# Kernel tuning notes

Measured on AMD Instinct MI355X. Metric: run time of the kernel, lower is better.

Reference implementation:

```python
import jax, jax.numpy as jnp
import numpy as np

N = 50000
E = 600000
F_IN = 128      # float features (in_channels - 1)
CE = 8          # cell embedding dim
D_IN = F_IN + CE  # 136
C = 128         # out_channels
NUM_CELLS = 854
NEG_SLOPE = 0.2
LN_EPS = 1e-5


def _gat_layer(x, src, dst, W, a_src, a_dst, b):
    """PyG GATConv, heads=1, concat=False, add_self_loops already in src/dst.
    x: [N, Din]; src/dst: [Etot]; W: [Din, C]; a_src/a_dst: [C]; b: [C].
    """
    h = x @ W                               # [N, C]
    alpha_src = h @ a_src                   # [N]
    alpha_dst = h @ a_dst                   # [N]
    e = jax.nn.leaky_relu(alpha_src[src] + alpha_dst[dst], NEG_SLOPE)  # [Etot]
    # segment softmax over edges sharing a destination node
    m = jax.ops.segment_max(e, dst, num_segments=N)    # [N] (every node has a self-loop)
    ex = jnp.exp(e - m[dst])                           # [Etot]
    denom = jax.ops.segment_sum(ex, dst, num_segments=N)  # [N]
    alpha = ex / denom[dst]                            # [Etot]
    out = jax.ops.segment_sum(h[src] * alpha[:, None], dst, num_segments=N)  # [N, C]
    return out + b


def _layer_norm(x, g, b):
    mu = jnp.mean(x, axis=-1, keepdims=True)
    var = jnp.var(x, axis=-1, keepdims=True)
    return (x - mu) * jax.lax.rsqrt(var + LN_EPS) * g + b


def setup_inputs() -> dict:
    key = jax.random.key(0)
    ks = jax.random.split(key, 12)
    x_base = jax.random.normal(ks[0], (N, F_IN), dtype=jnp.float32)
    cell_ids = jax.random.randint(ks[1], (N,), 0, NUM_CELLS, dtype=jnp.int64)
    edge_index = jax.random.randint(ks[2], (2, E), 0, N, dtype=jnp.int64)
    s = 0.05
    cell_emb = jax.random.normal(ks[3], (NUM_CELLS, CE), dtype=jnp.float32)
    W1 = jax.random.normal(ks[4], (D_IN, C), dtype=jnp.float32) * s
    a_src1 = jax.random.normal(ks[5], (C,), dtype=jnp.float32) * s
    a_dst1 = jax.random.normal(ks[6], (C,), dtype=jnp.float32) * s
    b1 = jnp.zeros((C,), dtype=jnp.float32)
    ln_g = jnp.ones((C,), dtype=jnp.float32)
    ln_b = jnp.zeros((C,), dtype=jnp.float32)
    W2 = jax.random.normal(ks[7], (C, C), dtype=jnp.float32) * s
    a_src2 = jax.random.normal(ks[8], (C,), dtype=jnp.float32) * s
    a_dst2 = jax.random.normal(ks[9], (C,), dtype=jnp.float32) * s
    b2 = jnp.zeros((C,), dtype=jnp.float32)
    return {
        "x_base": x_base, "cell_ids": cell_ids, "edge_index": edge_index,
        "cell_emb": cell_emb,
        "W1": W1, "a_src1": a_src1, "a_dst1": a_dst1, "b1": b1,
        "ln_g": ln_g, "ln_b": ln_b,
        "W2": W2, "a_src2": a_src2, "a_dst2": a_dst2, "b2": b2,
    }


def reference(x_base, cell_ids, edge_index, cell_emb,
              W1, a_src1, a_dst1, b1, ln_g, ln_b,
              W2, a_src2, a_dst2, b2):
    # embed cell ids and concat (equiv. to x[:, :-1] + Embedding(x[:, -1]))
    x = jnp.concatenate([x_base, cell_emb[cell_ids]], axis=1)   # [N, 136]
    # PyG GATConv adds self-loops internally
    loops = jnp.arange(N, dtype=edge_index.dtype)
    src = jnp.concatenate([edge_index[0], loops])
    dst = jnp.concatenate([edge_index[1], loops])
    # layer 1 + LN + ELU (dropout inactive in eval mode)
    x = _gat_layer(x, src, dst, W1, a_src1, a_dst1, b1)
    x = jax.nn.elu(_layer_norm(x, ln_g, ln_b))
    # layer 2 (no norm/activation on last layer)
    x = _gat_layer(x, src, dst, W2, a_src2, a_dst2, b2)
    return x
```

## Files before the change

kernel.cpp:

```cpp
#include <hip/hip_runtime.h>
#include <hip/hip_fp16.h>
#include <cstdint>
#include <cstddef>

#define NEG_SLOPE 0.2f
#define LN_EPS 1e-5f

constexpr int BS = 256;
constexpr int EPT = 8;
constexpr int STRIDE = 96;

typedef _Float16 f16x8 __attribute__((ext_vector_type(8)));
typedef float f32x4 __attribute__((ext_vector_type(4)));

__global__ __launch_bounds__(256) void k_init(
    int* __restrict__ cnt, unsigned short* __restrict__ sn,
    const float* __restrict__ W1, const float* __restrict__ W2,
    _Float16* __restrict__ Wt1, _Float16* __restrict__ Wt2,
    int n, int nbN)
{
    int b = blockIdx.x;
    if (b < nbN) {
        int i = b * BS + threadIdx.x;
        if (i < n) { cnt[i] = 1; sn[(size_t)i * STRIDE] = (unsigned short)i; }
    } else {
        int idx = (b - nbN) * BS + threadIdx.x;
        if (idx < 128 * 160) {
            int nn = idx / 160, k = idx - nn * 160;
            Wt1[idx] = (_Float16)((k < 136) ? W1[(size_t)k * 128 + nn] : 0.f);
        } else if (idx < 128 * 160 + 128 * 128) {
            int j = idx - 128 * 160;
            int nn = j >> 7, k = j & 127;
            Wt2[j] = (_Float16)W2[(size_t)k * 128 + nn];
        }
    }
}

__global__ __launch_bounds__(256) void k_scatter_gemm1(
    const int* __restrict__ esrc, const int* __restrict__ edst,
    int* __restrict__ cnt, unsigned short* __restrict__ sn,
    const float* __restrict__ x, const int* __restrict__ cid,
    const float* __restrict__ emb,
    const _Float16* __restrict__ Wt1,
    const float* __restrict__ a_src, const float* __restrict__ a_dst,
    _Float16* __restrict__ hb, float* __restrict__ as_, float* __restrict__ ad_,
    int e, int n, int nbG, int nbA)
{
    __shared__ float red[2][16][2][2];
    int b = blockIdx.x;
    int role, idx;
    int nInter = 2 * (nbG < nbA ? nbG : nbA);
    if (b < nInter)      { role = b & 1; idx = b >> 1; }
    else if (nbG < nbA)  { role = 1; idx = (b - nInter) + nbG; }
    else                 { role = 0; idx = (b - nInter) + nbA; }

    if (role == 1) {
        int base = idx * (BS * EPT) + threadIdx.x;
        int sv[EPT], dv[EPT], slot[EPT];
        #pragma unroll
        for (int u = 0; u < EPT; ++u) {
            int i = base + u * BS;
            bool ok = i < e;
            int ii = ok ? i : 0;
            sv[u] = esrc[ii];
            dv[u] = ok ? edst[ii] : -1;
        }
        #pragma unroll
        for (int u = 0; u < EPT; ++u)
            slot[u] = (dv[u] >= 0) ? atomicAdd(&cnt[dv[u]], 1) : STRIDE;
        #pragma unroll
        for (int u = 0; u < EPT; ++u)
            if (slot[u] < STRIDE)
                sn[(size_t)dv[u] * STRIDE + slot[u]] = (unsigned short)sv[u];
        return;
    }

    int tid = threadIdx.x;
    int wave = tid >> 6, lane = tid & 63;
    int rg = wave >> 1, ch = wave & 1;
    int r15 = lane & 15, q = lane >> 4;
    int rowBase = idx * 32 + rg * 16;
    int colBase = ch * 64;
    int row = rowBase + r15;
    bool ok = row < n;
    int rl = ok ? row : n - 1;

    f32x4 acc[4] = {};
    const _Float16* Wp[4];
    #pragma unroll
    for (int s = 0; s < 4; ++s)
        Wp[s] = Wt1 + (size_t)(colBase + s * 16 + r15) * 160 + q * 8;
    const float* Xp = x + (size_t)rl * 128 + q * 8;

    #pragma unroll
    for (int k0 = 0; k0 < 128; k0 += 32) {
        f16x8 wv[4];
        #pragma unroll
        for (int s = 0; s < 4; ++s) wv[s] = *(const f16x8*)(Wp[s] + k0);
        float4 xlo = *(const float4*)(Xp + k0);
        float4 xhi = *(const float4*)(Xp + k0 + 4);
        f16x8 xv;
        xv[0] = (_Float16)xlo.x; xv[1] = (_Float16)xlo.y;
        xv[2] = (_Float16)xlo.z; xv[3] = (_Float16)xlo.w;
        xv[4] = (_Float16)xhi.x; xv[5] = (_Float16)xhi.y;
        xv[6] = (_Float16)xhi.z; xv[7] = (_Float16)xhi.w;
        #pragma unroll
        for (int s = 0; s < 4; ++s)
            acc[s] = __builtin_amdgcn_mfma_f32_16x16x32_f16(wv[s], xv, acc[s], 0, 0, 0);
    }
    {
        f16x8 wv[4];
        #pragma unroll
        for (int s = 0; s < 4; ++s) wv[s] = *(const f16x8*)(Wp[s] + 128);
        f16x8 xv;
        #pragma unroll
        for (int j = 0; j < 8; ++j) xv[j] = (_Float16)0.f;
        if (q == 0) {
            const float* er = emb + (size_t)cid[rl] * 8;
            float4 e0 = *(const float4*)er;
            float4 e1 = *(const float4*)(er + 4);
            xv[0] = (_Float16)e0.x; xv[1] = (_Float16)e0.y;
            xv[2] = (_Float16)e0.z; xv[3] = (_Float16)e0.w;
            xv[4] = (_Float16)e1.x; xv[5] = (_Float16)e1.y;
            xv[6] = (_Float16)e1.z; xv[7] = (_Float16)e1.w;
        }
        #pragma unroll
        for (int s = 0; s < 4; ++s)
            acc[s] = __builtin_amdgcn_mfma_f32_16x16x32_f16(wv[s], xv, acc[s], 0, 0, 0);
    }

    float vs = 0.f, vd = 0.f;
    #pragma unroll
    for (int s = 0; s < 4; ++s) {
        float4 as4 = *(const float4*)&a_src[colBase + s * 16 + q * 4];
        float4 ad4 = *(const float4*)&a_dst[colBase + s * 16 + q * 4];
        f32x4 d = acc[s];
        vs += d[0]*as4.x + d[1]*as4.y + d[2]*as4.z + d[3]*as4.w;
        vd += d[0]*ad4.x + d[1]*ad4.y + d[2]*ad4.z + d[3]*ad4.w;
        if (ok) {
            ushort4 u;
            u.x = __half_as_ushort(__float2half_rn(d[0]));
            u.y = __half_as_ushort(__float2half_rn(d[1]));
            u.z = __half_as_ushort(__float2half_rn(d[2]));
            u.w = __half_as_ushort(__float2half_rn(d[3]));
            *(ushort4*)&hb[(size_t)row * 128 + colBase + s * 16 + q * 4] = u;
        }
    }
    vs += __shfl_xor(vs, 16); vs += __shfl_xor(vs, 32);
    vd += __shfl_xor(vd, 16); vd += __shfl_xor(vd, 32);
    if (q == 0) { red[rg][r15][ch][0] = vs; red[rg][r15][ch][1] = vd; }
    __syncthreads();
    if (ch == 0 && q == 0 && ok) {
        as_[row] = red[rg][r15][0][0] + red[rg][r15][1][0];
        ad_[row] = red[rg][r15][0][1] + red[rg][r15][1][1];
    }
}

__global__ __launch_bounds__(512, 8) void k_agg1_gemm2(
    const _Float16* __restrict__ h1, const unsigned short* __restrict__ sn,
    const int* __restrict__ cnt, const float* __restrict__ as1,
    const float* __restrict__ ad1, const float* __restrict__ b1,
    const float* __restrict__ lng, const float* __restrict__ lnb,
    const _Float16* __restrict__ Wt2,
    const float* __restrict__ a_src2, const float* __restrict__ a_dst2,
    _Float16* __restrict__ h2, float* __restrict__ as2, float* __restrict__ ad2,
    int nn)
{
    __shared__ _Float16 yt[32][144];
    __shared__ float red[2][16][4][2];
    int t = blockIdx.x;
    int tid = threadIdx.x;
    int wave = tid >> 6, lane = tid & 63;
    int l4 = lane & 15, q = lane >> 4;
    int qg = wave * 4 + q;
    int node = t * 32 + qg;
    bool valid = node < nn;
    const char* hbB = (const char*)h1;

    int len = 0; float adv = 0.f;
    if (valid) {
        len = cnt[node];
        len = len < STRIDE ? len : STRIDE;
        adv = ad1[node];
    }
    int start = node * STRIDE;
    int sub = l4 & 3;

    float acc[8] = {0.f, 0.f, 0.f, 0.f, 0.f, 0.f, 0.f, 0.f};
    float dsum = 0.f;
    for (int j = 0; j < len; j += 4) {
        int rem = len - j;
        unsigned long long s4 = *(const unsigned long long*)(sn + start + j);
        int my = (int)((s4 >> (sub * 16)) & 0xFFFFull);
        float tt = as1[my] + adv;
        tt = tt > 0.f ? tt : NEG_SLOPE * tt;
        float w = __expf(fminf(tt, 70.f));
        #pragma unroll
        for (int i = 0; i < 4; ++i) {
            if (i < rem) {
                int si = (int)((s4 >> (i * 16)) & 0xFFFFull);
                float wi = __shfl(w, (lane & 48) | i);
                f16x8 hv = *(const f16x8*)(hbB + ((size_t)si << 8) + l4 * 16);
                #pragma unroll
                for (int c = 0; c < 8; ++c)
                    acc[c] = fmaf(wi, (float)hv[c], acc[c]);
                dsum += wi;
            }
        }
    }

    if (valid) {
        float inv = 1.f / dsum;
        float4 b0 = *(const float4*)&b1[l4 * 8];
        float4 bb = *(const float4*)&b1[l4 * 8 + 4];
        float vv[8];
        vv[0] = acc[0] * inv + b0.x; vv[1] = acc[1] * inv + b0.y;
        vv[2] = acc[2] * inv + b0.z; vv[3] = acc[3] * inv + b0.w;
        vv[4] = acc[4] * inv + bb.x; vv[5] = acc[5] * inv + bb.y;
        vv[6] = acc[6] * inv + bb.z; vv[7] = acc[7] * inv + bb.w;

        float s1 = 0.f, s2 = 0.f;
        #pragma unroll
        for (int c = 0; c < 8; ++c) { s1 += vv[c]; s2 += vv[c] * vv[c]; }
        #pragma unroll
        for (int o = 1; o < 16; o <<= 1) {
            s1 += __shfl_xor(s1, o);
            s2 += __shfl_xor(s2, o);
        }
        float mean = s1 * (1.f / 128.f);
        float var  = s2 * (1.f / 128.f) - mean * mean;
        float r = rsqrtf(var + LN_EPS);
        float4 g0 = *(const float4*)&lng[l4 * 8];
        float4 g1 = *(const float4*)&lng[l4 * 8 + 4];
        float4 p0 = *(const float4*)&lnb[l4 * 8];
        float4 p1 = *(const float4*)&lnb[l4 * 8 + 4];
        float gg[8] = {g0.x, g0.y, g0.z, g0.w, g1.x, g1.y, g1.z, g1.w};
        float pp[8] = {p0.x, p0.y, p0.z, p0.w, p1.x, p1.y, p1.z, p1.w};
        f16x8 o;
        #pragma unroll
        for (int c = 0; c < 8; ++c) {
            float u = (vv[c] - mean) * r * gg[c] + pp[c];
            u = u > 0.f ? u : __expf(u) - 1.f;
            o[c] = (_Float16)u;
        }
        *(f16x8*)&yt[qg][l4 * 8] = o;
    } else {
        f16x8 z;
        #pragma unroll
        for (int c = 0; c < 8; ++c) z[c] = (_Float16)0.f;
        *(f16x8*)&yt[qg][l4 * 8] = z;
    }
    __syncthreads();

    int rg = wave >> 2, cc = wave & 3;
    int r15 = l4;
    int row = t * 32 + rg * 16 + r15;
    bool ok = row < nn;

    f32x4 acc2[2] = {};
    const _Float16* Wp[2];
    #pragma unroll
    for (int s = 0; s < 2; ++s)
        Wp[s] = Wt2 + (size_t)(cc * 32 + s * 16 + r15) * 128 + q * 8;
    const _Float16* Yp = &yt[rg * 16 + r15][q * 8];

    #pragma unroll
    for (int k0 = 0; k0 < 128; k0 += 32) {
        f16x8 wv[2];
        #pragma unroll
        for (int s = 0; s < 2; ++s) wv[s] = *(const f16x8*)(Wp[s] + k0);
        f16x8 xv = *(const f16x8*)(Yp + k0);
        #pragma unroll
        for (int s = 0; s < 2; ++s)
            acc2[s] = __builtin_amdgcn_mfma_f32_16x16x32_f16(wv[s], xv, acc2[s], 0, 0, 0);
    }

    float vs = 0.f, vd = 0.f;
    #pragma unroll
    for (int s = 0; s < 2; ++s) {
        float4 as4 = *(const float4*)&a_src2[cc * 32 + s * 16 + q * 4];
        float4 ad4 = *(const float4*)&a_dst2[cc * 32 + s * 16 + q * 4];
        f32x4 d = acc2[s];
        vs += d[0]*as4.x + d[1]*as4.y + d[2]*as4.z + d[3]*as4.w;
        vd += d[0]*ad4.x + d[1]*ad4.y + d[2]*ad4.z + d[3]*ad4.w;
        if (ok) {
            ushort4 u;
            u.x = __half_as_ushort(__float2half_rn(d[0]));
            u.y = __half_as_ushort(__float2half_rn(d[1]));
            u.z = __half_as_ushort(__float2half_rn(d[2]));
            u.w = __half_as_ushort(__float2half_rn(d[3]));
            *(ushort4*)&h2[(size_t)row * 128 + cc * 32 + s * 16 + q * 4] = u;
        }
    }
    vs += __shfl_xor(vs, 16); vs += __shfl_xor(vs, 32);
    vd += __shfl_xor(vd, 16); vd += __shfl_xor(vd, 32);
    if (q == 0) { red[rg][r15][cc][0] = vs; red[rg][r15][cc][1] = vd; }
    __syncthreads();
    if (cc == 0 && q == 0 && ok) {
        as2[row] = red[rg][r15][0][0] + red[rg][r15][1][0]
                 + red[rg][r15][2][0] + red[rg][r15][3][0];
        ad2[row] = red[rg][r15][0][1] + red[rg][r15][1][1]
                 + red[rg][r15][2][1] + red[rg][r15][3][1];
    }
}

__global__ __launch_bounds__(256) void k_agg2(
    const _Float16* __restrict__ hb, const unsigned short* __restrict__ sn,
    const int* __restrict__ cnt, const float* __restrict__ as_,
    const float* __restrict__ ad_, const float* __restrict__ bias,
    float* __restrict__ out, int n_nodes)
{
    int tid = threadIdx.x;
    int wave = tid >> 6, lane = tid & 63;
    int l4 = lane & 15, q = lane >> 4;
    int node = blockIdx.x * 16 + wave * 4 + q;
    if (node >= n_nodes) return;
    int len = cnt[node];
    len = len < STRIDE ? len : STRIDE;
    int start = node * STRIDE;
    int sub = l4 & 3;
    float adv = ad_[node];
    const char* hbB = (const char*)hb;

    float acc[8] = {0.f, 0.f, 0.f, 0.f, 0.f, 0.f, 0.f, 0.f};
    float dsum = 0.f;
    for (int j = 0; j < len; j += 4) {
        int rem = len - j;
        unsigned long long s4 = *(const unsigned long long*)(sn + start + j);
        int my = (int)((s4 >> (sub * 16)) & 0xFFFFull);
        float t = as_[my] + adv;
        t = t > 0.f ? t : NEG_SLOPE * t;
        float w = __expf(fminf(t, 70.f));
        #pragma unroll
        for (int i = 0; i < 4; ++i) {
            if (i < rem) {
                int si = (int)((s4 >> (i * 16)) & 0xFFFFull);
                float wi = __shfl(w, (lane & 48) | i);
                f16x8 hv = *(const f16x8*)(hbB + ((size_t)si << 8) + l4 * 16);
                #pragma unroll
                for (int c = 0; c < 8; ++c)
                    acc[c] = fmaf(wi, (float)hv[c], acc[c]);
                dsum += wi;
            }
        }
    }

    float inv = 1.f / dsum;
    float4 b0 = *(const float4*)&bias[l4 * 8];
    float4 b1 = *(const float4*)&bias[l4 * 8 + 4];
    float4 o0 = make_float4(acc[0]*inv + b0.x, acc[1]*inv + b0.y,
                            acc[2]*inv + b0.z, acc[3]*inv + b0.w);
    float4 o1 = make_float4(acc[4]*inv + b1.x, acc[5]*inv + b1.y,
                            acc[6]*inv + b1.z, acc[7]*inv + b1.w);
    *(float4*)(out + (size_t)node * 128 + l4 * 8)     = o0;
    *(float4*)(out + (size_t)node * 128 + l4 * 8 + 4) = o1;
}


extern "C" void kernel_launch(void* const* d_in, const int* in_sizes, int n_in,
                              void* d_out, int out_size, void* d_ws, size_t ws_size,
                              hipStream_t stream) {
    const float* x_base   = (const float*)d_in[0];
    const int*   cell_ids = (const int*)d_in[1];
    const int*   eidx     = (const int*)d_in[2];
    const float* cell_emb = (const float*)d_in[3];
    const float* W1     = (const float*)d_in[4];
    const float* a_src1 = (const float*)d_in[5];
    const float* a_dst1 = (const float*)d_in[6];
    const float* b1     = (const float*)d_in[7];
    const float* ln_g   = (const float*)d_in[8];
    const float* ln_b   = (const float*)d_in[9];
    const float* W2     = (const float*)d_in[10];
    const float* a_src2 = (const float*)d_in[11];
    const float* a_dst2 = (const float*)d_in[12];
    const float* b2     = (const float*)d_in[13];

    const int N = in_sizes[0] / 128;
    const int E = in_sizes[2] / 2;

    const int* esrc = eidx;
    const int* edst = eidx + E;

    auto align = [](size_t v) { return (v + 255) & ~(size_t)255; };
    char* p = (char*)d_ws;
    int*   cnt    = (int*)p;   p += align((size_t)N * 4);
    unsigned short* sn = (unsigned short*)p; p += align((size_t)N * STRIDE * 2 + 64);
    _Float16* h1  = (_Float16*)p; p += align((size_t)N * 128 * 2);
    _Float16* h2  = (_Float16*)p; p += align((size_t)N * 128 * 2);
    _Float16* Wt1 = (_Float16*)p; p += align((size_t)128 * 160 * 2);
    _Float16* Wt2 = (_Float16*)p; p += align((size_t)128 * 128 * 2);
    float* as1    = (float*)p; p += align((size_t)N * 4);
    float* ad1    = (float*)p; p += align((size_t)N * 4);
    float* as2    = (float*)p; p += align((size_t)N * 4);
    float* ad2    = (float*)p; p += align((size_t)N * 4);
    (void)ws_size; (void)n_in; (void)out_size;

    const int nbN = (N + BS - 1) / BS;
    const int nbA = (E + BS * EPT - 1) / (BS * EPT);
    const int nbG = (N + 31) / 32;
    const int wblocks = (128 * 160 + 128 * 128 + BS - 1) / BS;

    k_init<<<nbN + wblocks, BS, 0, stream>>>(cnt, sn, W1, W2, Wt1, Wt2, N, nbN);
    k_scatter_gemm1<<<nbG + nbA, BS, 0, stream>>>(
        esrc, edst, cnt, sn, x_base, cell_ids, cell_emb, Wt1,
        a_src1, a_dst1, h1, as1, ad1, E, N, nbG, nbA);
    k_agg1_gemm2<<<nbG, 512, 0, stream>>>(
        h1, sn, cnt, as1, ad1, b1, ln_g, ln_b, Wt2,
        a_src2, a_dst2, h2, as2, ad2, N);
    k_agg2<<<(N + 15) / 16, BS, 0, stream>>>(
        h2, sn, cnt, as2, ad2, b2, (float*)d_out, N);
}
```

Baseline: 222.1 us.

## Replace global-atomic edge scatter with two-pass bucketed CSR build using shared atomics

Edge-to-adjacency construction changes from one pass of global atomicAdd per edge into a two-pass bucket sort. The first pass bins edges by destination into 1024-node buckets per edge block using LDS atomics and writes packed (dst_local, src) words. The second pass has one block per bucket fill the per-node slot lists with shared-memory counters. This removes contended global atomics, but each sub-bucket is capped at 96 entries, so edges can be dropped silently if a block sends more than 96 edges to one bucket. Bucket-building blocks now run serially over about 293 sub-lists per bucket, which may become a long tail.

```diff
diff --git a/kernel.cpp b/kernel.cpp
--- a/kernel.cpp
+++ b/kernel.cpp
@@ -8,23 +8,49 @@
 
 constexpr int BS = 256;
 constexpr int EPT = 8;
+constexpr int SUBCAP = 96;
 constexpr int STRIDE = 96;
 
 typedef _Float16 f16x8 __attribute__((ext_vector_type(8)));
 typedef float f32x4 __attribute__((ext_vector_type(4)));
 
 __global__ __launch_bounds__(256) void k_init(
-    int* __restrict__ cnt, unsigned short* __restrict__ sn,
+    const int* __restrict__ esrc, const int* __restrict__ edst,
+    unsigned int* __restrict__ gb, int* __restrict__ bcnt,
     const float* __restrict__ W1, const float* __restrict__ W2,
     _Float16* __restrict__ Wt1, _Float16* __restrict__ Wt2,
-    int n, int nbN)
+    int e, int nb, int nblk)
 {
     int b = blockIdx.x;
-    if (b < nbN) {
-        int i = b * BS + threadIdx.x;
-        if (i < n) { cnt[i] = 1; sn[(size_t)i * STRIDE] = (unsigned short)i; }
+    if (b < nblk) {
+        __shared__ int lcnt[64];
+        int tid = threadIdx.x;
+        if (tid < 64) lcnt[tid] = 0;
+        __syncthreads();
+        int base = b * (BS * EPT) + tid;
+        int sv[EPT], dl[EPT], bk[EPT], lp[EPT];
+        #pragma unroll
+        for (int u = 0; u < EPT; ++u) {
+            int i = base + u * BS;
+            bool ok = i < e;
+            int ii = ok ? i : 0;
+            sv[u] = esrc[ii];
+            int d = edst[ii];
+            dl[u] = d & 1023;
+            bk[u] = ok ? (d >> 10) : -1;
+        }
+        #pragma unroll
+        for (int u = 0; u < EPT; ++u)
+            lp[u] = (bk[u] >= 0) ? atomicAdd(&lcnt[bk[u]], 1) : SUBCAP;
+        __syncthreads();
+        if (tid < nb) bcnt[b * nb + tid] = lcnt[tid] < SUBCAP ? lcnt[tid] : SUBCAP;
+        #pragma unroll
+        for (int u = 0; u < EPT; ++u)
+            if (bk[u] >= 0 && lp[u] < SUBCAP)
+                gb[((size_t)bk[u] * nblk + b) * SUBCAP + lp[u]] =
+                    ((unsigned)dl[u] << 16) | (unsigned)sv[u];
     } else {
-        int idx = (b - nbN) * BS + threadIdx.x;
+        int idx = (b - nblk) * BS + threadIdx.x;
         if (idx < 128 * 160) {
             int nn = idx / 160, k = idx - nn * 160;
             Wt1[idx] = (_Float16)((k < 136) ? W1[(size_t)k * 128 + nn] : 0.f);
@@ -36,45 +62,49 @@
     }
 }
 
-__global__ __launch_bounds__(256) void k_scatter_gemm1(
-    const int* __restrict__ esrc, const int* __restrict__ edst,
+__global__ __launch_bounds__(256) void k_csr_gemm1(
+    const unsigned int* __restrict__ gb, const int* __restrict__ bcnt,
     int* __restrict__ cnt, unsigned short* __restrict__ sn,
     const float* __restrict__ x, const int* __restrict__ cid,
     const float* __restrict__ emb,
     const _Float16* __restrict__ Wt1,
     const float* __restrict__ a_src, const float* __restrict__ a_dst,
     _Float16* __restrict__ hb, float* __restrict__ as_, float* __restrict__ ad_,
-    int e, int n, int nbG, int nbA)
+    int n, int nb, int nblk)
 {
     __shared__ float red[2][16][2][2];
+    __shared__ int cl[1024];
     int b = blockIdx.x;
-    int role, idx;
-    int nInter = 2 * (nbG < nbA ? nbG : nbA);
-    if (b < nInter)      { role = b & 1; idx = b >> 1; }
-    else if (nbG < nbA)  { role = 1; idx = (b - nInter) + nbG; }
-    else                 { role = 0; idx = (b - nInter) + nbA; }
-
-    if (role == 1) {
-        int base = idx * (BS * EPT) + threadIdx.x;
-        int sv[EPT], dv[EPT], slot[EPT];
-        #pragma unroll
-        for (int u = 0; u < EPT; ++u) {
-            int i = base + u * BS;
-            bool ok = i < e;
-            int ii = ok ? i : 0;
-            sv[u] = esrc[ii];
-            dv[u] = ok ? edst[ii] : -1;
-        }
-        #pragma unroll
-        for (int u = 0; u < EPT; ++u)
-            slot[u] = (dv[u] >= 0) ? atomicAdd(&cnt[dv[u]], 1) : STRIDE;
-        #pragma unroll
-        for (int u = 0; u < EPT; ++u)
-            if (slot[u] < STRIDE)
-                sn[(size_t)dv[u] * STRIDE + slot[u]] = (unsigned short)sv[u];
+
+    if (b < nb) {
+        int tid = threadIdx.x;
+        #pragma unroll 4
+        for (int i = tid; i < 1024; i += BS) cl[i] = 1;
+        __syncthreads();
+        for (int blk = tid; blk < nblk; blk += BS) {
+            int c = bcnt[blk * nb + b];
+            size_t gbase = ((size_t)b * nblk + blk) * SUBCAP;
+            for (int j = 0; j < c; ++j) {
+                unsigned pk = gb[gbase + j];
+                int dlocal = (int)(pk >> 16), s = (int)(pk & 0xFFFFu);
+                int slot = atomicAdd(&cl[dlocal], 1);
+                if (slot < STRIDE)
+                    sn[((size_t)(b * 1024 + dlocal)) * STRIDE + slot] = (unsigned short)s;
+            }
+        }
+        __syncthreads();
+        for (int i = tid; i < 1024; i += BS) {
+            int node = b * 1024 + i;
+            if (node < n) {
+                int c = cl[i];
+                cnt[node] = c < STRIDE ? c : STRIDE;
+                sn[(size_t)node * STRIDE] = (unsigned short)node;
+            }
+        }
         return;
     }
 
+    int idx = b - nb;
     int tid = threadIdx.x;
     int wave = tid >> 6, lane = tid & 63;
     int rg = wave >> 1, ch = wave & 1;
@@ -381,10 +411,15 @@
     const int* esrc = eidx;
     const int* edst = eidx + E;
 
+    const int NB   = (N + 1023) >> 10;
+    const int NBLK = (E + BS * EPT - 1) / (BS * EPT);
+
     auto align = [](size_t v) { return (v + 255) & ~(size_t)255; };
     char* p = (char*)d_ws;
     int*   cnt    = (int*)p;   p += align((size_t)N * 4);
     unsigned short* sn = (unsigned short*)p; p += align((size_t)N * STRIDE * 2 + 64);
+    unsigned int* gb = (unsigned int*)p; p += align((size_t)NB * NBLK * SUBCAP * 4);
+    int*   bcnt   = (int*)p;   p += align((size_t)NBLK * NB * 4);
     _Float16* h1  = (_Float16*)p; p += align((size_t)N * 128 * 2);
     _Float16* h2  = (_Float16*)p; p += align((size_t)N * 128 * 2);
     _Float16* Wt1 = (_Float16*)p; p += align((size_t)128 * 160 * 2);
@@ -395,15 +430,14 @@
     float* ad2    = (float*)p; p += align((size_t)N * 4);
     (void)ws_size; (void)n_in; (void)out_size;
 
-    const int nbN = (N + BS - 1) / BS;
-    const int nbA = (E + BS * EPT - 1) / (BS * EPT);
     const int nbG = (N + 31) / 32;
     const int wblocks = (128 * 160 + 128 * 128 + BS - 1) / BS;
 
-    k_init<<<nbN + wblocks, BS, 0, stream>>>(cnt, sn, W1, W2, Wt1, Wt2, N, nbN);
-    k_scatter_gemm1<<<nbG + nbA, BS, 0, stream>>>(
-        esrc, edst, cnt, sn, x_base, cell_ids, cell_emb, Wt1,
-        a_src1, a_dst1, h1, as1, ad1, E, N, nbG, nbA);
+    k_init<<<NBLK + wblocks, BS, 0, stream>>>(
+        esrc, edst, gb, bcnt, W1, W2, Wt1, Wt2, E, NB, NBLK);
+    k_csr_gemm1<<<NB + nbG, BS, 0, stream>>>(
+        gb, bcnt, cnt, sn, x_base, cell_ids, cell_emb, Wt1,
+        a_src1, a_dst1, h1, as1, ad1, N, NB, NBLK);
     k_agg1_gemm2<<<nbG, 512, 0, stream>>>(
         h1, sn, cnt, as1, ad1, b1, ln_g, ln_b, Wt2,
         a_src2, a_dst2, h2, as2, ad2, N);
```

After: 229.3 us. +3.2%, slower.
